# Kernel optimization log

Measured on AMD Instinct MI355X. Metric: run time of the kernel, lower is better.

Reference implementation:

```python
import jax, jax.numpy as jnp
import numpy as np
from jax import lax

B_, L_, D_ = 4, 512, 512          # batch, seq_len, in_dim (d_model)
HID, H2 = 512, 256                # hidden_dim, per-direction LSTM width
NL, DST, DCV, DIN, DTR = 3, 16, 4, 1024, 32  # layers, d_state, d_conv, d_inner, dt_rank


def _silu(x):
    return x * jax.nn.sigmoid(x)


def _layernorm(x, g, b):
    m = x.mean(-1, keepdims=True)
    v = x.var(-1, keepdims=True)
    return (x - m) / jnp.sqrt(v + 1e-5) * g + b


def _mamba(x, wi, cw, cb, xpw, dw, db, Alog, Dp, wo):
    # x: (B,L,D)
    Bsz, Ls, _ = x.shape
    xz = jnp.einsum('bld,ed->ble', x, wi)          # (B,L,2*DIN)
    xin, z = jnp.split(xz, 2, axis=-1)
    # causal depthwise conv1d (kernel DCV, left-padded)
    xpad = jnp.pad(xin, ((0, 0), (DCV - 1, 0), (0, 0)))
    u = cb + sum(xpad[:, k:k + Ls, :] * cw[:, k] for k in range(DCV))
    u = _silu(u)                                   # (B,L,DIN)
    xdbl = jnp.einsum('blc,ec->ble', u, xpw)       # (B,L,DTR+2*DST)
    dt_in = xdbl[..., :DTR]
    Bc = xdbl[..., DTR:DTR + DST]
    Cc = xdbl[..., DTR + DST:]
    dt = jax.nn.softplus(jnp.einsum('blr,cr->blc', dt_in, dw) + db)  # (B,L,DIN)
    A = -jnp.exp(Alog)                             # (DIN,DST), negative

    def step(h, inp):
        dt_t, B_t, C_t, u_t = inp                  # (B,DIN),(B,DST),(B,DST),(B,DIN)
        dA = jnp.exp(dt_t[..., None] * A)          # (B,DIN,DST)
        h = dA * h + (dt_t * u_t)[..., None] * B_t[:, None, :]
        y = jnp.einsum('bcn,bn->bc', h, C_t)
        return h, y

    h0 = jnp.zeros((Bsz, DIN, DST), x.dtype)
    _, ys = lax.scan(step, h0, (dt.transpose(1, 0, 2), Bc.transpose(1, 0, 2),
                                Cc.transpose(1, 0, 2), u.transpose(1, 0, 2)))
    y = ys.transpose(1, 0, 2) + u * Dp
    y = y * _silu(z)
    return jnp.einsum('blc,dc->bld', y, wo)


def _lstm_dir(x, wih, whh, bih, bhh, reverse):
    Bsz = x.shape[0]

    def step(carry, xt):
        h, c = carry
        g = xt @ wih.T + h @ whh.T + bih + bhh     # (B,4*H2), PyTorch gate order i,f,g,o
        i, f, gg, o = jnp.split(g, 4, axis=-1)
        c = jax.nn.sigmoid(f) * c + jax.nn.sigmoid(i) * jnp.tanh(gg)
        h = jax.nn.sigmoid(o) * jnp.tanh(c)
        return (h, c), h

    init = (jnp.zeros((Bsz, H2), x.dtype), jnp.zeros((Bsz, H2), x.dtype))
    _, hs = lax.scan(step, init, x.transpose(1, 0, 2), reverse=reverse)
    return hs.transpose(1, 0, 2)


def setup_inputs():
    key = jax.random.key(0)
    ks = jax.random.split(key, 16)
    rn = lambda k, s, sc=0.02: jax.random.normal(k, s, jnp.float32) * sc
    inp = {}
    inp['x'] = jax.random.normal(ks[0], (B_, L_, D_), jnp.float32)
    inp['in_proj_w'] = rn(ks[1], (NL, 2 * DIN, D_))
    inp['conv_w'] = rn(ks[2], (NL, DIN, DCV), 0.2)
    inp['conv_b'] = jnp.zeros((NL, DIN), jnp.float32)
    inp['x_proj_w'] = rn(ks[3], (NL, DTR + 2 * DST, DIN))
    inp['dt_proj_w'] = rn(ks[4], (NL, DIN, DTR), 0.1)
    inp['dt_proj_b'] = jnp.full((NL, DIN), -4.0, jnp.float32)
    inp['A_log'] = jnp.log(jnp.broadcast_to(jnp.arange(1, DST + 1, dtype=jnp.float32), (NL, DIN, DST)))
    inp['D_param'] = jnp.ones((NL, DIN), jnp.float32)
    inp['out_proj_w'] = rn(ks[5], (NL, D_, DIN))
    inp['ln_g'] = jnp.ones((NL, D_), jnp.float32)
    inp['ln_b'] = jnp.zeros((NL, D_), jnp.float32)
    inp['lstm_w_ih'] = rn(ks[6], (2, 4 * H2, D_), 0.05)
    inp['lstm_w_hh'] = rn(ks[7], (2, 4 * H2, H2), 0.05)
    inp['lstm_b_ih'] = jnp.zeros((2, 4 * H2), jnp.float32)
    inp['lstm_b_hh'] = jnp.zeros((2, 4 * H2), jnp.float32)
    inp['fusion_w'] = rn(ks[8], (HID, D_ + HID), 0.02)
    inp['fusion_b'] = jnp.zeros((HID,), jnp.float32)
    return inp


def reference(x, in_proj_w, conv_w, conv_b, x_proj_w, dt_proj_w, dt_proj_b, A_log,
              D_param, out_proj_w, ln_g, ln_b, lstm_w_ih, lstm_w_hh, lstm_b_ih,
              lstm_b_hh, fusion_w, fusion_b):
    m = x
    for i in range(NL):
        mo = _mamba(m, in_proj_w[i], conv_w[i], conv_b[i], x_proj_w[i],
                    dt_proj_w[i], dt_proj_b[i], A_log[i], D_param[i], out_proj_w[i])
        m = _layernorm(m + mo, ln_g[i], ln_b[i])
    lf = _lstm_dir(x, lstm_w_ih[0], lstm_w_hh[0], lstm_b_ih[0], lstm_b_hh[0], False)
    lb = _lstm_dir(x, lstm_w_ih[1], lstm_w_hh[1], lstm_b_ih[1], lstm_b_hh[1], True)
    comb = jnp.concatenate([m, lf, lb], axis=-1)   # (B,L,D_+HID)
    return comb @ fusion_w.T + fusion_b
```

## Files before the change

kernel.cpp:

```cpp
#include <hip/hip_runtime.h>
#include <math.h>

#define B_  4
#define L_  512
#define D_  512
#define DIN 1024
#define DST 16
#define DCV 4
#define DTR 32
#define NL  3
#define H2  256
#define LCH 64
#define NCH 8
#define WSC 0.28f

typedef _Float16 __f16;
typedef __f16 f16x2 __attribute__((ext_vector_type(2)));
typedef __f16 half8 __attribute__((ext_vector_type(8)));
typedef float f32x4v __attribute__((ext_vector_type(4)));
typedef unsigned uint4v __attribute__((ext_vector_type(4)));

__device__ __forceinline__ float fast_sigmoid(float x) { return 1.f / (1.f + __expf(-x)); }
__device__ __forceinline__ float fast_tanh(float x) { return 2.f / (1.f + __expf(-2.f * x)) - 1.f; }

__device__ __forceinline__ unsigned packf16(float a, float b) {
  f16x2 p; p.x = (__f16)a; p.y = (__f16)b;
  return __builtin_bit_cast(unsigned, p);
}
__device__ __forceinline__ int sdot4(unsigned a, unsigned b, int c) {
  return __builtin_amdgcn_sdot4((int)a, (int)b, c, false);
}
__device__ __forceinline__ int q8(float v) {
  float c = fmaxf(fminf(v, 127.f), -127.f);
  return (int)rintf(c);
}

template<int ACT, bool ACC, bool HOUT>
__global__ __launch_bounds__(256) void gemm_mfma_h(
    const __f16* __restrict__ A, const __f16* __restrict__ W, void* __restrict__ Cv,
    int M, int N, int K, int lda, int ldb, int ldc,
    const float* __restrict__ bias, const float* __restrict__ bias2)
{
  __shared__ uint4v As[1024];
  __shared__ uint4v Bs[1024];
  const int tid  = threadIdx.x;
  const int lane = tid & 63, wid = tid >> 6;
  const int wr = wid >> 1, wc = wid & 1;
  const int fr = lane & 15, fq = lane >> 4;
  const int m0 = blockIdx.y * 128, n0 = blockIdx.x * 128;
  const int srow = tid >> 3, skb = tid & 7;

  f32x4v acc[4][4] = {};
  for (int k0 = 0; k0 < K; k0 += 64) {
    const __f16* Ab = A + (size_t)m0 * lda + k0;
    const __f16* Bb = W + (size_t)n0 * ldb + k0;
    #pragma unroll
    for (int i = 0; i < 4; ++i) {
      int row = srow + i * 32;
      uint4v ap = *(const uint4v*)(Ab + (size_t)row * lda + skb * 8);
      uint4v bp = *(const uint4v*)(Bb + (size_t)row * ldb + skb * 8);
      As[row * 8 + (skb ^ (row & 7))] = ap;
      Bs[row * 8 + (skb ^ (row & 7))] = bp;
    }
    __syncthreads();
    #pragma unroll
    for (int ks = 0; ks < 2; ++ks) {
      half8 af[4], bf[4];
      #pragma unroll
      for (int mt = 0; mt < 4; ++mt) {
        int row = wr * 64 + mt * 16 + fr;
        int kb = ks * 4 + fq;
        af[mt] = __builtin_bit_cast(half8, As[row * 8 + (kb ^ (row & 7))]);
      }
      #pragma unroll
      for (int nt = 0; nt < 4; ++nt) {
        int row = wc * 64 + nt * 16 + fr;
        int kb = ks * 4 + fq;
        bf[nt] = __builtin_bit_cast(half8, Bs[row * 8 + (kb ^ (row & 7))]);
      }
      #pragma unroll
      for (int mt = 0; mt < 4; ++mt)
        #pragma unroll
        for (int nt = 0; nt < 4; ++nt)
          acc[mt][nt] = __builtin_amdgcn_mfma_f32_16x16x32_f16(af[mt], bf[nt], acc[mt][nt], 0, 0, 0);
    }
    __syncthreads();
  }
  float* C = (float*)Cv;
  __f16* Ch = (__f16*)Cv;
  #pragma unroll
  for (int nt = 0; nt < 4; ++nt) {
    int n = n0 + wc * 64 + nt * 16 + fr;
    float bv = (bias ? bias[n] : 0.f) + (bias2 ? bias2[n] : 0.f);
    #pragma unroll
    for (int mt = 0; mt < 4; ++mt) {
      #pragma unroll
      for (int r = 0; r < 4; ++r) {
        int m = m0 + wr * 64 + mt * 16 + fq * 4 + r;
        float v = acc[mt][nt][r] + bv;
        if (ACT == 1) v = (v > 20.f) ? v : log1pf(__expf(v));
        if (HOUT) Ch[(size_t)m * ldc + n] = (__f16)v;
        else if (ACC) C[(size_t)m * ldc + n] += v;
        else C[(size_t)m * ldc + n] = v;
      }
    }
  }
}

__global__ __launch_bounds__(256) void packh(
    const float* __restrict__ src, __f16* __restrict__ dst, int n)
{
  int t = blockIdx.x * 256 + threadIdx.x;
  if (t < n) dst[t] = (__f16)src[t];
}

__global__ __launch_bounds__(256) void pack_xpw_h(
    const float* __restrict__ xpw, __f16* __restrict__ dst)
{
  int t = blockIdx.x * 256 + threadIdx.x;
  int layer = t >> 17;
  int r = (t >> 10) & 127;
  int k = t & 1023;
  dst[t] = (r < 64) ? (__f16)xpw[layer * 65536 + r * 1024 + k] : (__f16)0.f;
}

__global__ __launch_bounds__(256) void pack_dwh(
    const float* __restrict__ dw, __f16* __restrict__ dst)
{
  int t = blockIdx.x * 256 + threadIdx.x;
  int layer = t >> 16;
  int r = (t >> 6) & 1023;
  int k = t & 63;
  dst[t] = (k < 32) ? (__f16)dw[layer * 32768 + r * 32 + k] : (__f16)0.f;
}

__global__ __launch_bounds__(256) void pack_whh_i8(
    const float* __restrict__ whh, uint4* __restrict__ dst)
{
  int idx = blockIdx.x * 256 + threadIdx.x;
  int t = idx & 511;
  int q = (idx >> 9) & 7;
  int r = idx >> 12;
  int G = r & 3, dir = r >> 2;
  int j = t >> 1, ks = t & 1;
  const float* src = whh + (size_t)dir * 262144 + (size_t)(G * 256 + j) * 256 + ks * 128 + q * 16;
  const float inv = 127.f / WSC;
  unsigned d[4];
  #pragma unroll
  for (int w = 0; w < 4; ++w) {
    float4 f = ((const float4*)src)[w];
    int q0 = q8(f.x * inv), q1 = q8(f.y * inv), q2 = q8(f.z * inv), q3 = q8(f.w * inv);
    d[w] = (unsigned)(q0 & 255) | ((unsigned)(q1 & 255) << 8) |
           ((unsigned)(q2 & 255) << 16) | ((unsigned)(q3 & 255) << 24);
  }
  uint4 pk; pk.x = d[0]; pk.y = d[1]; pk.z = d[2]; pk.w = d[3];
  dst[idx] = pk;
}

__global__ __launch_bounds__(256) void conv_silu(
    const float* __restrict__ xz, const float* __restrict__ cw, const float* __restrict__ cb,
    float* __restrict__ u, __f16* __restrict__ uh)
{
  int t = blockIdx.x * 256 + threadIdx.x;
  int c  = t & (DIN - 1);
  int bl = t >> 10;
  int l  = bl & (L_ - 1);
  float acc = cb[c];
  #pragma unroll
  for (int k = 0; k < DCV; ++k) {
    int ls = l + k - (DCV - 1);
    if (ls >= 0)
      acc = fmaf(xz[(size_t)(bl + k - (DCV - 1)) * 2048 + c], cw[c * DCV + k], acc);
  }
  float v = acc * fast_sigmoid(acc);
  u[t] = v;
  uh[t] = (__f16)v;
}

__global__ __launch_bounds__(256) void scan_part(
    const float* __restrict__ dt, const float* __restrict__ u,
    const __f16* __restrict__ xdh, const float* __restrict__ A_log,
    float* __restrict__ hend, float* __restrict__ Pp)
{
  int t = blockIdx.x * 256 + threadIdx.x;
  int n  = t & 15;
  int ch = (t >> 4) & 7;
  int bc = t >> 7;
  int c  = bc & (DIN - 1);
  int b  = bc >> 10;
  float Ac = -__expf(A_log[c * DST + n]);
  float h = 0.f, P = 1.f;
  const size_t row = (size_t)b * L_ + ch * LCH;

#define DECLP(i) float dtv##i, uv##i, Bn##i;
  DECLP(0) DECLP(1) DECLP(2) DECLP(3)
#define LOADP(i, l) { \
    const size_t nb_ = row + (l); \
    dtv##i = dt[nb_ * DIN + c]; \
    uv##i  = u [nb_ * DIN + c]; \
    Bn##i  = (float)xdh[nb_ * 128 + 32 + n]; }
#define STEPP(i) { \
    float dA_ = __expf(dtv##i * Ac); \
    h = fmaf(dA_, h, (dtv##i * uv##i) * Bn##i); \
    P *= dA_; }

  LOADP(0, 0) LOADP(1, 1) LOADP(2, 2) LOADP(3, 3)
  for (int l = 0; l < LCH - 4; l += 4) {
    STEPP(0) LOADP(0, l + 4)
    STEPP(1) LOADP(1, l + 5)
    STEPP(2) LOADP(2, l + 6)
    STEPP(3) LOADP(3, l + 7)
  }
  STEPP(0) STEPP(1) STEPP(2) STEPP(3)
#undef DECLP
#undef LOADP
#undef STEPP
  int flat = bc * 16 + n;
  hend[ch * 65536 + flat] = h;
  Pp[ch * 65536 + flat]   = P;
}

__global__ __launch_bounds__(256) void scan_fix(
    const float* __restrict__ dt, const float* __restrict__ u,
    const __f16* __restrict__ xdh, const float* __restrict__ xz,
    const float* __restrict__ A_log, const float* __restrict__ Dp,
    const float* __restrict__ hend, const float* __restrict__ Pp,
    __f16* __restrict__ y)
{
  int t = blockIdx.x * 256 + threadIdx.x;
  int n  = t & 15;
  int ch = (t >> 4) & 7;
  int bc = t >> 7;
  int c  = bc & (DIN - 1);
  int b  = bc >> 10;
  float Ac = -__expf(A_log[c * DST + n]);
  float Dc = Dp[c];
  const int flat = bc * 16 + n;
  float h = 0.f;
  for (int c2 = 0; c2 < ch; ++c2)
    h = fmaf(Pp[c2 * 65536 + flat], h, hend[c2 * 65536 + flat]);
  const size_t row = (size_t)b * L_ + ch * LCH;

#define DECLP(i) float dtv##i, uv##i, Bn##i, Cn##i, zv##i;
  DECLP(0) DECLP(1) DECLP(2) DECLP(3)
#define LOADP(i, l) { \
    const size_t nb_ = row + (l); \
    dtv##i = dt[nb_ * DIN + c]; \
    uv##i  = u [nb_ * DIN + c]; \
    Bn##i  = (float)xdh[nb_ * 128 + 32 + n]; \
    Cn##i  = (float)xdh[nb_ * 128 + 48 + n]; \
    zv##i  = xz[nb_ * 2048 + 1024 + c]; }
#define STEPP(i, l) { \
    float dA_ = __expf(dtv##i * Ac); \
    h = fmaf(dA_, h, (dtv##i * uv##i) * Bn##i); \
    float p_ = h * Cn##i; \
    p_ += __shfl_xor(p_, 1, 64); \
    p_ += __shfl_xor(p_, 2, 64); \
    p_ += __shfl_xor(p_, 4, 64); \
    p_ += __shfl_xor(p_, 8, 64); \
    if (n == 0) { \
      float yv_ = p_ + uv##i * Dc; \
      yv_ *= zv##i * fast_sigmoid(zv##i); \
      y[(row + (l)) * DIN + c] = (__f16)yv_; \
    } }

  LOADP(0, 0) LOADP(1, 1) LOADP(2, 2) LOADP(3, 3)
  for (int l = 0; l < LCH - 4; l += 4) {
    STEPP(0, l)     LOADP(0, l + 4)
    STEPP(1, l + 1) LOADP(1, l + 5)
    STEPP(2, l + 2) LOADP(2, l + 6)
    STEPP(3, l + 3) LOADP(3, l + 7)
  }
  STEPP(0, LCH - 4) STEPP(1, LCH - 3) STEPP(2, LCH - 2) STEPP(3, LCH - 1)
#undef DECLP
#undef LOADP
#undef STEPP
}

__global__ __launch_bounds__(64) void resid_ln(
    const float* __restrict__ a, const float* __restrict__ mo,
    const float* __restrict__ g, const float* __restrict__ bta,
    float* __restrict__ outm, int ldo, __f16* __restrict__ outh, int ldoh)
{
  int row = blockIdx.x;
  int lane = threadIdx.x;
  const float* pa = a  + (size_t)row * 512;
  const float* pb = mo + (size_t)row * 512;
  float v[8];
  float s = 0.f, s2 = 0.f;
  #pragma unroll
  for (int i = 0; i < 8; ++i) {
    float x = pa[lane + i * 64] + pb[lane + i * 64];
    v[i] = x; s += x; s2 += x * x;
  }
  #pragma unroll
  for (int off = 1; off < 64; off <<= 1) {
    s  += __shfl_xor(s,  off, 64);
    s2 += __shfl_xor(s2, off, 64);
  }
  float mean = s * (1.f / 512.f);
  float var  = s2 * (1.f / 512.f) - mean * mean;
  float rstd = rsqrtf(var + 1e-5f);
  #pragma unroll
  for (int i = 0; i < 8; ++i) {
    int cidx = lane + i * 64;
    float o = (v[i] - mean) * rstd * g[cidx] + bta[cidx];
    if (outm) outm[(size_t)row * ldo + cidx] = o;
    outh[(size_t)row * ldoh + cidx] = (__f16)o;
  }
}


#define W8STEP(q) { \
    uint4 hq = h8s[buf][(q)*2 + ks]; \
    uint4 wi_ = wp8[(0*8+(q))*512 + t]; \
    uint4 wf_ = wp8[(1*8+(q))*512 + t]; \
    uint4 wg = wg_lds[(q)*512 + t]; \
    uint4 wo = wo_lds[(q)*512 + t]; \
    ii_ = sdot4(wi_.x, hq.x, ii_); ii_ = sdot4(wi_.y, hq.y, ii_); \
    ii_ = sdot4(wi_.z, hq.z, ii_); ii_ = sdot4(wi_.w, hq.w, ii_); \
    if_ = sdot4(wf_.x, hq.x, if_); if_ = sdot4(wf_.y, hq.y, if_); \
    if_ = sdot4(wf_.z, hq.z, if_); if_ = sdot4(wf_.w, hq.w, if_); \
    ig_ = sdot4(wg.x, hq.x, ig_); ig_ = sdot4(wg.y, hq.y, ig_); \
    ig_ = sdot4(wg.z, hq.z, ig_); ig_ = sdot4(wg.w, hq.w, ig_); \
    io_ = sdot4(wo.x, hq.x, io_); io_ = sdot4(wo.y, hq.y, io_); \
    io_ = sdot4(wo.z, hq.z, io_); io_ = sdot4(wo.w, hq.w, io_); }
#define REP8(M) M(0) M(1) M(2) M(3) M(4) M(5) M(6) M(7)

__global__ __launch_bounds__(512, 1) void lstm_rec(
    const float* __restrict__ gx, const uint4* __restrict__ wpk8,
    __f16* __restrict__ comb)
{
  __shared__ uint4 wg_lds[8 * 512];
  __shared__ uint4 wo_lds[8 * 512];
  __shared__ __align__(16) uint4 h8s[2][16];
  const int dir = blockIdx.x >> 2, b = blockIdx.x & 3;
  const int t = threadIdx.x;
  const int j = t >> 1, ks = t & 1;
  const uint4* wp8 = wpk8 + (size_t)dir * 4 * 8 * 512;
  const float WS = WSC / (127.f * 127.f);

  #pragma unroll
  for (int q = 0; q < 8; ++q) {
    wg_lds[q * 512 + t] = wp8[(2 * 8 + q) * 512 + t];
    wo_lds[q * 512 + t] = wp8[(3 * 8 + q) * 512 + t];
  }

  if (t < 128) ((unsigned*)h8s)[t] = 0u;
  float c_reg = 0.f;
  __f16* outp = comb + 512 + dir * 256;
  const float* gxb = gx + (size_t)(b * L_) * 2048 + dir * 1024;
  const int offA = (ks ? 1 : 0) * 256 + j;
  const int offB = (ks ? 3 : 2) * 256 + j;
  const int d_   = t >> 3;
  const int ks8  = d_ >> 5;
  const int h8i  = (((d_ - ks8 * 32) >> 2) * 2 + ks8) * 4 + (d_ & 3);
  __syncthreads();

  int buf = 0;
  const int l0 = dir ? (L_ - 1) : 0;
  float pgA = gxb[(size_t)l0 * 2048 + offA];
  float pgB = gxb[(size_t)l0 * 2048 + offB];

  for (int s = 0; s < L_; ++s) {
    const int l = dir ? (L_ - 1 - s) : s;
    float pgA_n = 0.f, pgB_n = 0.f;
    if (s + 1 < L_) {
      const int ln = dir ? (L_ - 2 - s) : (s + 1);
      pgA_n = gxb[(size_t)ln * 2048 + offA];
      pgB_n = gxb[(size_t)ln * 2048 + offB];
    }
    int ii_ = 0, if_ = 0, ig_ = 0, io_ = 0;
    REP8(W8STEP)
    float a0 = (float)ii_ * WS;
    float a1 = (float)if_ * WS;
    float a2 = (float)ig_ * WS;
    float a3 = (float)io_ * WS;
    if (ks == 0) { a0 += pgA; a2 += pgB; } else { a1 += pgA; a3 += pgB; }
    a0 += __shfl_xor(a0, 1, 64);
    a1 += __shfl_xor(a1, 1, 64);
    a2 += __shfl_xor(a2, 1, 64);
    a3 += __shfl_xor(a3, 1, 64);
    const float si = fast_sigmoid(a0);
    const float sf = fast_sigmoid(a1);
    const float tg = fast_tanh(a2);
    const float so = fast_sigmoid(a3);
    c_reg = fmaf(sf, c_reg, si * tg);
    const float hv = so * fast_tanh(c_reg);
    if (ks == 0) outp[(size_t)(b * L_ + l) * 1024 + j] = (__f16)hv;
    const float hv1 = __shfl_xor(hv, 2, 64);
    const float hv2 = __shfl_xor(hv, 4, 64);
    const float hv3 = __shfl_xor(hv1, 4, 64);
    if ((t & 7) == 0) {
      int q0 = (int)rintf(hv  * 127.f), q1 = (int)rintf(hv1 * 127.f);
      int q2 = (int)rintf(hv2 * 127.f), q3 = (int)rintf(hv3 * 127.f);
      ((unsigned*)h8s[buf ^ 1])[h8i] =
          (unsigned)(q0 & 255) | ((unsigned)(q1 & 255) << 8) |
          ((unsigned)(q2 & 255) << 16) | ((unsigned)(q3 & 255) << 24);
    }
    pgA = pgA_n; pgB = pgB_n;
    buf ^= 1;
    __syncthreads();
  }
}

extern "C" void kernel_launch(void* const* d_in, const int* in_sizes, int n_in,
                              void* d_out, int out_size, void* d_ws, size_t ws_size,
                              hipStream_t stream)
{
  const float* x    = (const float*)d_in[0];
  const float* wi   = (const float*)d_in[1];
  const float* cw   = (const float*)d_in[2];
  const float* cb   = (const float*)d_in[3];
  const float* xpw  = (const float*)d_in[4];
  const float* dw   = (const float*)d_in[5];
  const float* db   = (const float*)d_in[6];
  const float* Alog = (const float*)d_in[7];
  const float* Dp   = (const float*)d_in[8];
  const float* wo   = (const float*)d_in[9];
  const float* lng  = (const float*)d_in[10];
  const float* lnb  = (const float*)d_in[11];
  const float* wih  = (const float*)d_in[12];
  const float* whh  = (const float*)d_in[13];
  const float* bih  = (const float*)d_in[14];
  const float* bhh  = (const float*)d_in[15];
  const float* fw   = (const float*)d_in[16];
  const float* fb   = (const float*)d_in[17];
  float* out = (float*)d_out;

  float* F = (float*)d_ws;
  float* xz     = F;
  float* gx     = F;
  float* mo     = F + 3145728;
  float* u      = F + 4194304;
  __f16* xdh    = (__f16*)(F + 7340032);
  float* dt     = F + 7602176;
  float* mbuf   = F + 10747904;
  __f16* fw_h   = (__f16*)(F + 4194304);
  __f16* u_h    = (__f16*)(F + 6291456);
  __f16* wih_h  = (__f16*)(F + 7602176);
  uint4* wpk8   = (uint4*)(F + 8126464);
  __f16* wi_hc  = (__f16*)(F + 8388608);
  float* hend   = F + 8388608;
  __f16* ybuf_h = (__f16*)(F + 9699328);
  __f16* x_h    = (__f16*)(F + 9699328);
  __f16* mbuf_h = (__f16*)(F + 11796480);
  float* Pp     = F + 11796480;
  __f16* comb_h = (__f16*)(F + 12320768);
  __f16* wo_h   = (__f16*)(F + 13369344);
  __f16* xpw_h  = (__f16*)(F + 14155776);
  __f16* dwh    = (__f16*)(F + 14352384);

  const int M = B_ * L_;
  dim3 blk(256);

  packh<<<dim3(4096), blk, 0, stream>>>(x,   x_h,   1048576);
  packh<<<dim3(4096), blk, 0, stream>>>(wih, wih_h, 1048576);
  packh<<<dim3(6144), blk, 0, stream>>>(wo,  wo_h,  1572864);
  pack_xpw_h<<<dim3(1536), blk, 0, stream>>>(xpw, xpw_h);
  pack_dwh<<<dim3(768), blk, 0, stream>>>(dw, dwh);

  gemm_mfma_h<0,false,false><<<dim3(16, 16), blk, 0, stream>>>(
      x_h, wih_h, gx, M, 2048, 512, 512, 512, 2048, bih, bhh);
  pack_whh_i8<<<dim3(128), blk, 0, stream>>>(whh, wpk8);
  lstm_rec<<<dim3(8), dim3(512), 0, stream>>>(gx, wpk8, comb_h);

  for (int i = 0; i < NL; ++i) {
    const float* min = (i == 0) ? x : mbuf;
    const __f16* min_h = (i == 0) ? x_h : mbuf_h;
    packh<<<dim3(4096), blk, 0, stream>>>(wi + (size_t)i*1048576, wi_hc, 1048576);
    gemm_mfma_h<0,false,false><<<dim3(16, 16), blk, 0, stream>>>(
        min_h, wi_hc, xz, M, 2048, 512, 512, 512, 2048, nullptr, nullptr);
    conv_silu<<<dim3(8192), blk, 0, stream>>>(
        xz, cw + (size_t)i*DIN*DCV, cb + i*DIN, u, u_h);
    gemm_mfma_h<0,false,true><<<dim3(1, 16), blk, 0, stream>>>(
        u_h, xpw_h + (size_t)i*131072, xdh, M, 128, 1024, 1024, 1024, 128, nullptr, nullptr);
    gemm_mfma_h<1,false,false><<<dim3(8, 16), blk, 0, stream>>>(
        xdh, dwh + (size_t)i*65536, dt, M, 1024, 64, 128, 64, 1024, db + i*1024, nullptr);
    scan_part<<<dim3(2048), blk, 0, stream>>>(
        dt, u, xdh, Alog + (size_t)i*DIN*DST, hend, Pp);
    scan_fix<<<dim3(2048), blk, 0, stream>>>(
        dt, u, xdh, xz, Alog + (size_t)i*DIN*DST, Dp + i*DIN, hend, Pp, ybuf_h);
    gemm_mfma_h<0,false,false><<<dim3(4, 16), blk, 0, stream>>>(
        ybuf_h, wo_h + (size_t)i*524288, mo, M, 512, 1024, 1024, 1024, 512, nullptr, nullptr);
    if (i < NL - 1)
      resid_ln<<<dim3(M), dim3(64), 0, stream>>>(
          min, mo, lng + i*512, lnb + i*512, mbuf, 512, mbuf_h, 512);
    else
      resid_ln<<<dim3(M), dim3(64), 0, stream>>>(
          min, mo, lng + i*512, lnb + i*512, nullptr, 0, comb_h, 1024);
  }

  packh<<<dim3(2048), blk, 0, stream>>>(fw, fw_h, 524288);
  gemm_mfma_h<0,false,false><<<dim3(4, 16), blk, 0, stream>>>(
      comb_h, fw_h, out, M, 512, 1024, 1024, 1024, 512, fb, nullptr);
}
```

Measured before the change: 1.273 ms.

## Split LSTM recurrence into segments co-scheduled inside Mamba GEMM launches

The serial LSTM recurrence, previously its own 8-block kernel, is split into 512 steps spread across 12 segments. Each segment runs as extra blocks appended to one of the Mamba GEMM launches, so the recurrence overlaps the GEMM tiles. The GEMMs become a 512-thread kernel computing two tiles per block, and LSTM c/h state is carried through global memory between launches. The input-gate projection and u are now stored as fp16, cutting bandwidth at some cost in precision. The added risk is per-segment cost to reload weights into LDS, plus the ordering assumption that launches on one stream run sequentially.

```diff
diff --git a/kernel.cpp b/kernel.cpp
--- a/kernel.cpp
+++ b/kernel.cpp
@@ -11,7 +11,6 @@
 #define NL  3
 #define H2  256
 #define LCH 64
-#define NCH 8
 #define WSC 0.28f
 
 typedef _Float16 __f16;
@@ -35,284 +34,46 @@
   return (int)rintf(c);
 }
 
-template<int ACT, bool ACC, bool HOUT>
-__global__ __launch_bounds__(256) void gemm_mfma_h(
-    const __f16* __restrict__ A, const __f16* __restrict__ W, void* __restrict__ Cv,
-    int M, int N, int K, int lda, int ldb, int ldc,
-    const float* __restrict__ bias, const float* __restrict__ bias2)
-{
-  __shared__ uint4v As[1024];
-  __shared__ uint4v Bs[1024];
-  const int tid  = threadIdx.x;
-  const int lane = tid & 63, wid = tid >> 6;
-  const int wr = wid >> 1, wc = wid & 1;
-  const int fr = lane & 15, fq = lane >> 4;
-  const int m0 = blockIdx.y * 128, n0 = blockIdx.x * 128;
-  const int srow = tid >> 3, skb = tid & 7;
-
-  f32x4v acc[4][4] = {};
-  for (int k0 = 0; k0 < K; k0 += 64) {
-    const __f16* Ab = A + (size_t)m0 * lda + k0;
-    const __f16* Bb = W + (size_t)n0 * ldb + k0;
-    #pragma unroll
-    for (int i = 0; i < 4; ++i) {
-      int row = srow + i * 32;
-      uint4v ap = *(const uint4v*)(Ab + (size_t)row * lda + skb * 8);
-      uint4v bp = *(const uint4v*)(Bb + (size_t)row * ldb + skb * 8);
-      As[row * 8 + (skb ^ (row & 7))] = ap;
-      Bs[row * 8 + (skb ^ (row & 7))] = bp;
-    }
-    __syncthreads();
-    #pragma unroll
-    for (int ks = 0; ks < 2; ++ks) {
-      half8 af[4], bf[4];
-      #pragma unroll
-      for (int mt = 0; mt < 4; ++mt) {
-        int row = wr * 64 + mt * 16 + fr;
-        int kb = ks * 4 + fq;
-        af[mt] = __builtin_bit_cast(half8, As[row * 8 + (kb ^ (row & 7))]);
-      }
-      #pragma unroll
-      for (int nt = 0; nt < 4; ++nt) {
-        int row = wc * 64 + nt * 16 + fr;
-        int kb = ks * 4 + fq;
-        bf[nt] = __builtin_bit_cast(half8, Bs[row * 8 + (kb ^ (row & 7))]);
-      }
-      #pragma unroll
-      for (int mt = 0; mt < 4; ++mt)
-        #pragma unroll
-        for (int nt = 0; nt < 4; ++nt)
-          acc[mt][nt] = __builtin_amdgcn_mfma_f32_16x16x32_f16(af[mt], bf[nt], acc[mt][nt], 0, 0, 0);
-    }
-    __syncthreads();
-  }
-  float* C = (float*)Cv;
-  __f16* Ch = (__f16*)Cv;
-  #pragma unroll
-  for (int nt = 0; nt < 4; ++nt) {
-    int n = n0 + wc * 64 + nt * 16 + fr;
-    float bv = (bias ? bias[n] : 0.f) + (bias2 ? bias2[n] : 0.f);
-    #pragma unroll
-    for (int mt = 0; mt < 4; ++mt) {
-      #pragma unroll
-      for (int r = 0; r < 4; ++r) {
-        int m = m0 + wr * 64 + mt * 16 + fq * 4 + r;
-        float v = acc[mt][nt][r] + bv;
-        if (ACT == 1) v = (v > 20.f) ? v : log1pf(__expf(v));
-        if (HOUT) Ch[(size_t)m * ldc + n] = (__f16)v;
-        else if (ACC) C[(size_t)m * ldc + n] += v;
-        else C[(size_t)m * ldc + n] = v;
-      }
-    }
-  }
-}
-
-__global__ __launch_bounds__(256) void packh(
-    const float* __restrict__ src, __f16* __restrict__ dst, int n)
-{
-  int t = blockIdx.x * 256 + threadIdx.x;
-  if (t < n) dst[t] = (__f16)src[t];
-}
-
-__global__ __launch_bounds__(256) void pack_xpw_h(
-    const float* __restrict__ xpw, __f16* __restrict__ dst)
-{
-  int t = blockIdx.x * 256 + threadIdx.x;
-  int layer = t >> 17;
-  int r = (t >> 10) & 127;
-  int k = t & 1023;
-  dst[t] = (r < 64) ? (__f16)xpw[layer * 65536 + r * 1024 + k] : (__f16)0.f;
-}
-
-__global__ __launch_bounds__(256) void pack_dwh(
-    const float* __restrict__ dw, __f16* __restrict__ dst)
-{
-  int t = blockIdx.x * 256 + threadIdx.x;
-  int layer = t >> 16;
-  int r = (t >> 6) & 1023;
-  int k = t & 63;
-  dst[t] = (k < 32) ? (__f16)dw[layer * 32768 + r * 32 + k] : (__f16)0.f;
-}
-
-__global__ __launch_bounds__(256) void pack_whh_i8(
-    const float* __restrict__ whh, uint4* __restrict__ dst)
-{
-  int idx = blockIdx.x * 256 + threadIdx.x;
-  int t = idx & 511;
-  int q = (idx >> 9) & 7;
-  int r = idx >> 12;
-  int G = r & 3, dir = r >> 2;
-  int j = t >> 1, ks = t & 1;
-  const float* src = whh + (size_t)dir * 262144 + (size_t)(G * 256 + j) * 256 + ks * 128 + q * 16;
-  const float inv = 127.f / WSC;
-  unsigned d[4];
-  #pragma unroll
-  for (int w = 0; w < 4; ++w) {
-    float4 f = ((const float4*)src)[w];
-    int q0 = q8(f.x * inv), q1 = q8(f.y * inv), q2 = q8(f.z * inv), q3 = q8(f.w * inv);
-    d[w] = (unsigned)(q0 & 255) | ((unsigned)(q1 & 255) << 8) |
-           ((unsigned)(q2 & 255) << 16) | ((unsigned)(q3 & 255) << 24);
-  }
-  uint4 pk; pk.x = d[0]; pk.y = d[1]; pk.z = d[2]; pk.w = d[3];
-  dst[idx] = pk;
-}
-
-__global__ __launch_bounds__(256) void conv_silu(
-    const float* __restrict__ xz, const float* __restrict__ cw, const float* __restrict__ cb,
-    float* __restrict__ u, __f16* __restrict__ uh)
-{
-  int t = blockIdx.x * 256 + threadIdx.x;
-  int c  = t & (DIN - 1);
-  int bl = t >> 10;
-  int l  = bl & (L_ - 1);
-  float acc = cb[c];
-  #pragma unroll
-  for (int k = 0; k < DCV; ++k) {
-    int ls = l + k - (DCV - 1);
-    if (ls >= 0)
-      acc = fmaf(xz[(size_t)(bl + k - (DCV - 1)) * 2048 + c], cw[c * DCV + k], acc);
-  }
-  float v = acc * fast_sigmoid(acc);
-  u[t] = v;
-  uh[t] = (__f16)v;
-}
-
-__global__ __launch_bounds__(256) void scan_part(
-    const float* __restrict__ dt, const float* __restrict__ u,
-    const __f16* __restrict__ xdh, const float* __restrict__ A_log,
-    float* __restrict__ hend, float* __restrict__ Pp)
-{
-  int t = blockIdx.x * 256 + threadIdx.x;
-  int n  = t & 15;
-  int ch = (t >> 4) & 7;
-  int bc = t >> 7;
-  int c  = bc & (DIN - 1);
-  int b  = bc >> 10;
-  float Ac = -__expf(A_log[c * DST + n]);
-  float h = 0.f, P = 1.f;
-  const size_t row = (size_t)b * L_ + ch * LCH;
-
-#define DECLP(i) float dtv##i, uv##i, Bn##i;
-  DECLP(0) DECLP(1) DECLP(2) DECLP(3)
-#define LOADP(i, l) { \
-    const size_t nb_ = row + (l); \
-    dtv##i = dt[nb_ * DIN + c]; \
-    uv##i  = u [nb_ * DIN + c]; \
-    Bn##i  = (float)xdh[nb_ * 128 + 32 + n]; }
-#define STEPP(i) { \
-    float dA_ = __expf(dtv##i * Ac); \
-    h = fmaf(dA_, h, (dtv##i * uv##i) * Bn##i); \
-    P *= dA_; }
-
-  LOADP(0, 0) LOADP(1, 1) LOADP(2, 2) LOADP(3, 3)
-  for (int l = 0; l < LCH - 4; l += 4) {
-    STEPP(0) LOADP(0, l + 4)
-    STEPP(1) LOADP(1, l + 5)
-    STEPP(2) LOADP(2, l + 6)
-    STEPP(3) LOADP(3, l + 7)
-  }
-  STEPP(0) STEPP(1) STEPP(2) STEPP(3)
-#undef DECLP
-#undef LOADP
-#undef STEPP
-  int flat = bc * 16 + n;
-  hend[ch * 65536 + flat] = h;
-  Pp[ch * 65536 + flat]   = P;
-}
-
-__global__ __launch_bounds__(256) void scan_fix(
-    const float* __restrict__ dt, const float* __restrict__ u,
-    const __f16* __restrict__ xdh, const float* __restrict__ xz,
-    const float* __restrict__ A_log, const float* __restrict__ Dp,
-    const float* __restrict__ hend, const float* __restrict__ Pp,
-    __f16* __restrict__ y)
-{
-  int t = blockIdx.x * 256 + threadIdx.x;
-  int n  = t & 15;
-  int ch = (t >> 4) & 7;
-  int bc = t >> 7;
-  int c  = bc & (DIN - 1);
-  int b  = bc >> 10;
-  float Ac = -__expf(A_log[c * DST + n]);
-  float Dc = Dp[c];
-  const int flat = bc * 16 + n;
-  float h = 0.f;
-  for (int c2 = 0; c2 < ch; ++c2)
-    h = fmaf(Pp[c2 * 65536 + flat], h, hend[c2 * 65536 + flat]);
-  const size_t row = (size_t)b * L_ + ch * LCH;
-
-#define DECLP(i) float dtv##i, uv##i, Bn##i, Cn##i, zv##i;
-  DECLP(0) DECLP(1) DECLP(2) DECLP(3)
-#define LOADP(i, l) { \
-    const size_t nb_ = row + (l); \
-    dtv##i = dt[nb_ * DIN + c]; \
-    uv##i  = u [nb_ * DIN + c]; \
-    Bn##i  = (float)xdh[nb_ * 128 + 32 + n]; \
-    Cn##i  = (float)xdh[nb_ * 128 + 48 + n]; \
-    zv##i  = xz[nb_ * 2048 + 1024 + c]; }
-#define STEPP(i, l) { \
-    float dA_ = __expf(dtv##i * Ac); \
-    h = fmaf(dA_, h, (dtv##i * uv##i) * Bn##i); \
-    float p_ = h * Cn##i; \
-    p_ += __shfl_xor(p_, 1, 64); \
-    p_ += __shfl_xor(p_, 2, 64); \
-    p_ += __shfl_xor(p_, 4, 64); \
-    p_ += __shfl_xor(p_, 8, 64); \
-    if (n == 0) { \
-      float yv_ = p_ + uv##i * Dc; \
-      yv_ *= zv##i * fast_sigmoid(zv##i); \
-      y[(row + (l)) * DIN + c] = (__f16)yv_; \
-    } }
-
-  LOADP(0, 0) LOADP(1, 1) LOADP(2, 2) LOADP(3, 3)
-  for (int l = 0; l < LCH - 4; l += 4) {
-    STEPP(0, l)     LOADP(0, l + 4)
-    STEPP(1, l + 1) LOADP(1, l + 5)
-    STEPP(2, l + 2) LOADP(2, l + 6)
-    STEPP(3, l + 3) LOADP(3, l + 7)
-  }
-  STEPP(0, LCH - 4) STEPP(1, LCH - 3) STEPP(2, LCH - 2) STEPP(3, LCH - 1)
-#undef DECLP
-#undef LOADP
-#undef STEPP
-}
-
-__global__ __launch_bounds__(64) void resid_ln(
-    const float* __restrict__ a, const float* __restrict__ mo,
-    const float* __restrict__ g, const float* __restrict__ bta,
-    float* __restrict__ outm, int ldo, __f16* __restrict__ outh, int ldoh)
-{
-  int row = blockIdx.x;
-  int lane = threadIdx.x;
-  const float* pa = a  + (size_t)row * 512;
-  const float* pb = mo + (size_t)row * 512;
-  float v[8];
-  float s = 0.f, s2 = 0.f;
-  #pragma unroll
-  for (int i = 0; i < 8; ++i) {
-    float x = pa[lane + i * 64] + pb[lane + i * 64];
-    v[i] = x; s += x; s2 += x * x;
-  }
-  #pragma unroll
-  for (int off = 1; off < 64; off <<= 1) {
-    s  += __shfl_xor(s,  off, 64);
-    s2 += __shfl_xor(s2, off, 64);
-  }
-  float mean = s * (1.f / 512.f);
-  float var  = s2 * (1.f / 512.f) - mean * mean;
-  float rstd = rsqrtf(var + 1e-5f);
-  #pragma unroll
-  for (int i = 0; i < 8; ++i) {
-    int cidx = lane + i * 64;
-    float o = (v[i] - mean) * rstd * g[cidx] + bta[cidx];
-    if (outm) outm[(size_t)row * ldo + cidx] = o;
-    outh[(size_t)row * ldoh + cidx] = (__f16)o;
-  }
-}
-
+__device__ void lstm_seg(char* smem, const __f16* gxh, const uint4* wpk8,
+                         __f16* comb, float* c_state, uint4* h8_state,
+                         int s0, int s1, int lb)
+{
+  uint4* wg_lds = (uint4*)smem;
+  uint4* wo_lds = wg_lds + 8 * 512;
+  uint4* h8s    = wo_lds + 8 * 512;
+  const int dir = lb >> 2, b = lb & 3;
+  const int t = threadIdx.x;
+  const int j = t >> 1, ks = t & 1;
+  const uint4* wp8 = wpk8 + (size_t)dir * 4 * 8 * 512;
+  const float WS = WSC / (127.f * 127.f);
+
+  #pragma unroll
+  for (int q = 0; q < 8; ++q) {
+    wg_lds[q * 512 + t] = wp8[(2 * 8 + q) * 512 + t];
+    wo_lds[q * 512 + t] = wp8[(3 * 8 + q) * 512 + t];
+  }
+  int buf = s0 & 1;
+  if (s0 == 0) {
+    if (t < 128) ((unsigned*)h8s)[t] = 0u;
+  } else {
+    if (t < 64) ((unsigned*)h8s)[buf * 64 + t] = ((const unsigned*)(h8_state + lb * 16))[t];
+  }
+  float c_reg = (s0 == 0) ? 0.f : c_state[lb * 512 + t];
+  __f16* outp = comb + 512 + dir * 256;
+  const __f16* gxb = gxh + (size_t)(b * L_) * 2048 + dir * 1024;
+  const int offA = (ks ? 1 : 0) * 256 + j;
+  const int offB = (ks ? 3 : 2) * 256 + j;
+  const int d_   = t >> 3;
+  const int ks8  = d_ >> 5;
+  const int h8i  = (((d_ - ks8 * 32) >> 2) * 2 + ks8) * 4 + (d_ & 3);
+  __syncthreads();
+
+  const int l00 = dir ? (L_ - 1 - s0) : s0;
+  float pgA = (float)gxb[(size_t)l00 * 2048 + offA];
+  float pgB = (float)gxb[(size_t)l00 * 2048 + offB];
 
 #define W8STEP(q) { \
-    uint4 hq = h8s[buf][(q)*2 + ks]; \
+    uint4 hq = h8s[buf * 16 + (q) * 2 + ks]; \
     uint4 wi_ = wp8[(0*8+(q))*512 + t]; \
     uint4 wf_ = wp8[(1*8+(q))*512 + t]; \
     uint4 wg = wg_lds[(q)*512 + t]; \
@@ -325,53 +86,18 @@
     ig_ = sdot4(wg.z, hq.z, ig_); ig_ = sdot4(wg.w, hq.w, ig_); \
     io_ = sdot4(wo.x, hq.x, io_); io_ = sdot4(wo.y, hq.y, io_); \
     io_ = sdot4(wo.z, hq.z, io_); io_ = sdot4(wo.w, hq.w, io_); }
-#define REP8(M) M(0) M(1) M(2) M(3) M(4) M(5) M(6) M(7)
-
-__global__ __launch_bounds__(512, 1) void lstm_rec(
-    const float* __restrict__ gx, const uint4* __restrict__ wpk8,
-    __f16* __restrict__ comb)
-{
-  __shared__ uint4 wg_lds[8 * 512];
-  __shared__ uint4 wo_lds[8 * 512];
-  __shared__ __align__(16) uint4 h8s[2][16];
-  const int dir = blockIdx.x >> 2, b = blockIdx.x & 3;
-  const int t = threadIdx.x;
-  const int j = t >> 1, ks = t & 1;
-  const uint4* wp8 = wpk8 + (size_t)dir * 4 * 8 * 512;
-  const float WS = WSC / (127.f * 127.f);
-
-  #pragma unroll
-  for (int q = 0; q < 8; ++q) {
-    wg_lds[q * 512 + t] = wp8[(2 * 8 + q) * 512 + t];
-    wo_lds[q * 512 + t] = wp8[(3 * 8 + q) * 512 + t];
-  }
-
-  if (t < 128) ((unsigned*)h8s)[t] = 0u;
-  float c_reg = 0.f;
-  __f16* outp = comb + 512 + dir * 256;
-  const float* gxb = gx + (size_t)(b * L_) * 2048 + dir * 1024;
-  const int offA = (ks ? 1 : 0) * 256 + j;
-  const int offB = (ks ? 3 : 2) * 256 + j;
-  const int d_   = t >> 3;
-  const int ks8  = d_ >> 5;
-  const int h8i  = (((d_ - ks8 * 32) >> 2) * 2 + ks8) * 4 + (d_ & 3);
-  __syncthreads();
-
-  int buf = 0;
-  const int l0 = dir ? (L_ - 1) : 0;
-  float pgA = gxb[(size_t)l0 * 2048 + offA];
-  float pgB = gxb[(size_t)l0 * 2048 + offB];
-
-  for (int s = 0; s < L_; ++s) {
+
+  for (int s = s0; s < s1; ++s) {
     const int l = dir ? (L_ - 1 - s) : s;
     float pgA_n = 0.f, pgB_n = 0.f;
     if (s + 1 < L_) {
       const int ln = dir ? (L_ - 2 - s) : (s + 1);
-      pgA_n = gxb[(size_t)ln * 2048 + offA];
-      pgB_n = gxb[(size_t)ln * 2048 + offB];
+      pgA_n = (float)gxb[(size_t)ln * 2048 + offA];
+      pgB_n = (float)gxb[(size_t)ln * 2048 + offB];
     }
     int ii_ = 0, if_ = 0, ig_ = 0, io_ = 0;
-    REP8(W8STEP)
+    W8STEP(0) W8STEP(1) W8STEP(2) W8STEP(3)
+    W8STEP(4) W8STEP(5) W8STEP(6) W8STEP(7)
     float a0 = (float)ii_ * WS;
     float a1 = (float)if_ * WS;
     float a2 = (float)ig_ * WS;
@@ -394,13 +120,372 @@
     if ((t & 7) == 0) {
       int q0 = (int)rintf(hv  * 127.f), q1 = (int)rintf(hv1 * 127.f);
       int q2 = (int)rintf(hv2 * 127.f), q3 = (int)rintf(hv3 * 127.f);
-      ((unsigned*)h8s[buf ^ 1])[h8i] =
+      ((unsigned*)(h8s + (buf ^ 1) * 16))[h8i] =
           (unsigned)(q0 & 255) | ((unsigned)(q1 & 255) << 8) |
           ((unsigned)(q2 & 255) << 16) | ((unsigned)(q3 & 255) << 24);
     }
     pgA = pgA_n; pgB = pgB_n;
     buf ^= 1;
     __syncthreads();
+  }
+#undef W8STEP
+  if (t < 64) ((unsigned*)(h8_state + lb * 16))[t] = ((unsigned*)(h8s + (s1 & 1) * 16))[t];
+  c_state[lb * 512 + t] = c_reg;
+}
+
+template<int ACT, bool HOUT>
+__global__ __launch_bounds__(512, 1) void gemm512(
+    const __f16* __restrict__ A, const __f16* __restrict__ W, void* __restrict__ Cv,
+    int nx, int M, int N, int K, int lda, int ldb, int ldc,
+    const float* __restrict__ bias,
+    int tileBlocks,
+    const __f16* __restrict__ gxh, const uint4* __restrict__ wpk8,
+    __f16* __restrict__ comb, float* __restrict__ c_state, uint4* __restrict__ h8_state,
+    int s0, int s1)
+{
+  extern __shared__ char smem[];
+  if ((int)blockIdx.x >= tileBlocks) {
+    lstm_seg(smem, gxh, wpk8, comb, c_state, h8_state, s0, s1, (int)blockIdx.x - tileBlocks);
+    return;
+  }
+  const int half = threadIdx.x >> 8;
+  const int tid  = threadIdx.x & 255;
+  const int tile = (int)blockIdx.x * 2 + half;
+  const int tx = tile % nx, ty = tile / nx;
+  uint4v* As = (uint4v*)(smem + half * 32768);
+  uint4v* Bs = As + 1024;
+  const int lane = tid & 63, wid = tid >> 6;
+  const int wr = wid >> 1, wc = wid & 1;
+  const int fr = lane & 15, fq = lane >> 4;
+  const int m0 = ty * 128, n0 = tx * 128;
+  const int srow = tid >> 3, skb = tid & 7;
+
+  f32x4v acc[4][4] = {};
+  for (int k0 = 0; k0 < K; k0 += 64) {
+    const __f16* Ab = A + (size_t)m0 * lda + k0;
+    const __f16* Bb = W + (size_t)n0 * ldb + k0;
+    #pragma unroll
+    for (int i = 0; i < 4; ++i) {
+      int row = srow + i * 32;
+      uint4v ap = *(const uint4v*)(Ab + (size_t)row * lda + skb * 8);
+      uint4v bp = *(const uint4v*)(Bb + (size_t)row * ldb + skb * 8);
+      As[row * 8 + (skb ^ (row & 7))] = ap;
+      Bs[row * 8 + (skb ^ (row & 7))] = bp;
+    }
+    __syncthreads();
+    #pragma unroll
+    for (int ks = 0; ks < 2; ++ks) {
+      half8 af[4], bf[4];
+      #pragma unroll
+      for (int mt = 0; mt < 4; ++mt) {
+        int row = wr * 64 + mt * 16 + fr;
+        int kb = ks * 4 + fq;
+        af[mt] = __builtin_bit_cast(half8, As[row * 8 + (kb ^ (row & 7))]);
+      }
+      #pragma unroll
+      for (int nt = 0; nt < 4; ++nt) {
+        int row = wc * 64 + nt * 16 + fr;
+        int kb = ks * 4 + fq;
+        bf[nt] = __builtin_bit_cast(half8, Bs[row * 8 + (kb ^ (row & 7))]);
+      }
+      #pragma unroll
+      for (int mt = 0; mt < 4; ++mt)
+        #pragma unroll
+        for (int nt = 0; nt < 4; ++nt)
+          acc[mt][nt] = __builtin_amdgcn_mfma_f32_16x16x32_f16(af[mt], bf[nt], acc[mt][nt], 0, 0, 0);
+    }
+    __syncthreads();
+  }
+  float* C = (float*)Cv;
+  __f16* Ch = (__f16*)Cv;
+  #pragma unroll
+  for (int nt = 0; nt < 4; ++nt) {
+    int n = n0 + wc * 64 + nt * 16 + fr;
+    float bv = bias ? bias[n] : 0.f;
+    #pragma unroll
+    for (int mt = 0; mt < 4; ++mt) {
+      #pragma unroll
+      for (int r = 0; r < 4; ++r) {
+        int m = m0 + wr * 64 + mt * 16 + fq * 4 + r;
+        float v = acc[mt][nt][r] + bv;
+        if (ACT == 1) v = (v > 20.f) ? v : log1pf(__expf(v));
+        if (HOUT) Ch[(size_t)m * ldc + n] = (__f16)v;
+        else C[(size_t)m * ldc + n] = v;
+      }
+    }
+  }
+}
+
+template<int ACT, bool HOUT>
+__global__ __launch_bounds__(256) void gemm_mfma_h(
+    const __f16* __restrict__ A, const __f16* __restrict__ W, void* __restrict__ Cv,
+    int M, int N, int K, int lda, int ldb, int ldc,
+    const float* __restrict__ bias, const float* __restrict__ bias2)
+{
+  __shared__ uint4v As[1024];
+  __shared__ uint4v Bs[1024];
+  const int tid  = threadIdx.x;
+  const int lane = tid & 63, wid = tid >> 6;
+  const int wr = wid >> 1, wc = wid & 1;
+  const int fr = lane & 15, fq = lane >> 4;
+  const int m0 = blockIdx.y * 128, n0 = blockIdx.x * 128;
+  const int srow = tid >> 3, skb = tid & 7;
+
+  f32x4v acc[4][4] = {};
+  for (int k0 = 0; k0 < K; k0 += 64) {
+    const __f16* Ab = A + (size_t)m0 * lda + k0;
+    const __f16* Bb = W + (size_t)n0 * ldb + k0;
+    #pragma unroll
+    for (int i = 0; i < 4; ++i) {
+      int row = srow + i * 32;
+      uint4v ap = *(const uint4v*)(Ab + (size_t)row * lda + skb * 8);
+      uint4v bp = *(const uint4v*)(Bb + (size_t)row * ldb + skb * 8);
+      As[row * 8 + (skb ^ (row & 7))] = ap;
+      Bs[row * 8 + (skb ^ (row & 7))] = bp;
+    }
+    __syncthreads();
+    #pragma unroll
+    for (int ks = 0; ks < 2; ++ks) {
+      half8 af[4], bf[4];
+      #pragma unroll
+      for (int mt = 0; mt < 4; ++mt) {
+        int row = wr * 64 + mt * 16 + fr;
+        int kb = ks * 4 + fq;
+        af[mt] = __builtin_bit_cast(half8, As[row * 8 + (kb ^ (row & 7))]);
+      }
+      #pragma unroll
+      for (int nt = 0; nt < 4; ++nt) {
+        int row = wc * 64 + nt * 16 + fr;
+        int kb = ks * 4 + fq;
+        bf[nt] = __builtin_bit_cast(half8, Bs[row * 8 + (kb ^ (row & 7))]);
+      }
+      #pragma unroll
+      for (int mt = 0; mt < 4; ++mt)
+        #pragma unroll
+        for (int nt = 0; nt < 4; ++nt)
+          acc[mt][nt] = __builtin_amdgcn_mfma_f32_16x16x32_f16(af[mt], bf[nt], acc[mt][nt], 0, 0, 0);
+    }
+    __syncthreads();
+  }
+  float* C = (float*)Cv;
+  __f16* Ch = (__f16*)Cv;
+  #pragma unroll
+  for (int nt = 0; nt < 4; ++nt) {
+    int n = n0 + wc * 64 + nt * 16 + fr;
+    float bv = (bias ? bias[n] : 0.f) + (bias2 ? bias2[n] : 0.f);
+    #pragma unroll
+    for (int mt = 0; mt < 4; ++mt) {
+      #pragma unroll
+      for (int r = 0; r < 4; ++r) {
+        int m = m0 + wr * 64 + mt * 16 + fq * 4 + r;
+        float v = acc[mt][nt][r] + bv;
+        if (ACT == 1) v = (v > 20.f) ? v : log1pf(__expf(v));
+        if (HOUT) Ch[(size_t)m * ldc + n] = (__f16)v;
+        else C[(size_t)m * ldc + n] = v;
+      }
+    }
+  }
+}
+
+__global__ __launch_bounds__(256) void packh(
+    const float* __restrict__ src, __f16* __restrict__ dst, int n)
+{
+  int t = blockIdx.x * 256 + threadIdx.x;
+  if (t < n) dst[t] = (__f16)src[t];
+}
+
+__global__ __launch_bounds__(256) void pack_xpw_h(
+    const float* __restrict__ xpw, __f16* __restrict__ dst)
+{
+  int t = blockIdx.x * 256 + threadIdx.x;
+  int layer = t >> 17;
+  int r = (t >> 10) & 127;
+  int k = t & 1023;
+  dst[t] = (r < 64) ? (__f16)xpw[layer * 65536 + r * 1024 + k] : (__f16)0.f;
+}
+
+__global__ __launch_bounds__(256) void pack_dwh(
+    const float* __restrict__ dw, __f16* __restrict__ dst)
+{
+  int t = blockIdx.x * 256 + threadIdx.x;
+  int layer = t >> 16;
+  int r = (t >> 6) & 1023;
+  int k = t & 63;
+  dst[t] = (k < 32) ? (__f16)dw[layer * 32768 + r * 32 + k] : (__f16)0.f;
+}
+
+__global__ __launch_bounds__(256) void pack_whh_i8(
+    const float* __restrict__ whh, uint4* __restrict__ dst)
+{
+  int idx = blockIdx.x * 256 + threadIdx.x;
+  int t = idx & 511;
+  int q = (idx >> 9) & 7;
+  int r = idx >> 12;
+  int G = r & 3, dir = r >> 2;
+  int j = t >> 1, ks = t & 1;
+  const float* src = whh + (size_t)dir * 262144 + (size_t)(G * 256 + j) * 256 + ks * 128 + q * 16;
+  const float inv = 127.f / WSC;
+  unsigned d[4];
+  #pragma unroll
+  for (int w = 0; w < 4; ++w) {
+    float4 f = ((const float4*)src)[w];
+    int q0 = q8(f.x * inv), q1 = q8(f.y * inv), q2 = q8(f.z * inv), q3 = q8(f.w * inv);
+    d[w] = (unsigned)(q0 & 255) | ((unsigned)(q1 & 255) << 8) |
+           ((unsigned)(q2 & 255) << 16) | ((unsigned)(q3 & 255) << 24);
+  }
+  uint4 pk; pk.x = d[0]; pk.y = d[1]; pk.z = d[2]; pk.w = d[3];
+  dst[idx] = pk;
+}
+
+__global__ __launch_bounds__(256) void conv_silu(
+    const float* __restrict__ xz, const float* __restrict__ cw, const float* __restrict__ cb,
+    __f16* __restrict__ uh)
+{
+  int t = blockIdx.x * 256 + threadIdx.x;
+  int c  = t & (DIN - 1);
+  int bl = t >> 10;
+  int l  = bl & (L_ - 1);
+  float acc = cb[c];
+  #pragma unroll
+  for (int k = 0; k < DCV; ++k) {
+    int ls = l + k - (DCV - 1);
+    if (ls >= 0)
+      acc = fmaf(xz[(size_t)(bl + k - (DCV - 1)) * 2048 + c], cw[c * DCV + k], acc);
+  }
+  float v = acc * fast_sigmoid(acc);
+  uh[t] = (__f16)v;
+}
+
+__global__ __launch_bounds__(256) void scan_part(
+    const float* __restrict__ dt, const __f16* __restrict__ uh,
+    const __f16* __restrict__ xdh, const float* __restrict__ A_log,
+    float* __restrict__ hend, float* __restrict__ Pp)
+{
+  int t = blockIdx.x * 256 + threadIdx.x;
+  int n  = t & 15;
+  int ch = (t >> 4) & 7;
+  int bc = t >> 7;
+  int c  = bc & (DIN - 1);
+  int b  = bc >> 10;
+  float Ac = -__expf(A_log[c * DST + n]);
+  float h = 0.f, P = 1.f;
+  const size_t row = (size_t)b * L_ + ch * LCH;
+
+#define DECLP(i) float dtv##i, uv##i, Bn##i;
+  DECLP(0) DECLP(1) DECLP(2) DECLP(3)
+#define LOADP(i, l) { \
+    const size_t nb_ = row + (l); \
+    dtv##i = dt[nb_ * DIN + c]; \
+    uv##i  = (float)uh[nb_ * DIN + c]; \
+    Bn##i  = (float)xdh[nb_ * 128 + 32 + n]; }
+#define STEPP(i) { \
+    float dA_ = __expf(dtv##i * Ac); \
+    h = fmaf(dA_, h, (dtv##i * uv##i) * Bn##i); \
+    P *= dA_; }
+
+  LOADP(0, 0) LOADP(1, 1) LOADP(2, 2) LOADP(3, 3)
+  for (int l = 0; l < LCH - 4; l += 4) {
+    STEPP(0) LOADP(0, l + 4)
+    STEPP(1) LOADP(1, l + 5)
+    STEPP(2) LOADP(2, l + 6)
+    STEPP(3) LOADP(3, l + 7)
+  }
+  STEPP(0) STEPP(1) STEPP(2) STEPP(3)
+#undef DECLP
+#undef LOADP
+#undef STEPP
+  int flat = bc * 16 + n;
+  hend[ch * 65536 + flat] = h;
+  Pp[ch * 65536 + flat]   = P;
+}
+
+__global__ __launch_bounds__(256) void scan_fix(
+    const float* __restrict__ dt, const __f16* __restrict__ uh,
+    const __f16* __restrict__ xdh, const float* __restrict__ xz,
+    const float* __restrict__ A_log, const float* __restrict__ Dp,
+    const float* __restrict__ hend, const float* __restrict__ Pp,
+    __f16* __restrict__ y)
+{
+  int t = blockIdx.x * 256 + threadIdx.x;
+  int n  = t & 15;
+  int ch = (t >> 4) & 7;
+  int bc = t >> 7;
+  int c  = bc & (DIN - 1);
+  int b  = bc >> 10;
+  float Ac = -__expf(A_log[c * DST + n]);
+  float Dc = Dp[c];
+  const int flat = bc * 16 + n;
+  float h = 0.f;
+  for (int c2 = 0; c2 < ch; ++c2)
+    h = fmaf(Pp[c2 * 65536 + flat], h, hend[c2 * 65536 + flat]);
+  const size_t row = (size_t)b * L_ + ch * LCH;
+
+#define DECLP(i) float dtv##i, uv##i, Bn##i, Cn##i, zv##i;
+  DECLP(0) DECLP(1) DECLP(2) DECLP(3)
+#define LOADP(i, l) { \
+    const size_t nb_ = row + (l); \
+    dtv##i = dt[nb_ * DIN + c]; \
+    uv##i  = (float)uh[nb_ * DIN + c]; \
+    Bn##i  = (float)xdh[nb_ * 128 + 32 + n]; \
+    Cn##i  = (float)xdh[nb_ * 128 + 48 + n]; \
+    zv##i  = xz[nb_ * 2048 + 1024 + c]; }
+#define STEPP(i, l) { \
+    float dA_ = __expf(dtv##i * Ac); \
+    h = fmaf(dA_, h, (dtv##i * uv##i) * Bn##i); \
+    float p_ = h * Cn##i; \
+    p_ += __shfl_xor(p_, 1, 64); \
+    p_ += __shfl_xor(p_, 2, 64); \
+    p_ += __shfl_xor(p_, 4, 64); \
+    p_ += __shfl_xor(p_, 8, 64); \
+    if (n == 0) { \
+      float yv_ = p_ + uv##i * Dc; \
+      yv_ *= zv##i * fast_sigmoid(zv##i); \
+      y[(row + (l)) * DIN + c] = (__f16)yv_; \
+    } }
+
+  LOADP(0, 0) LOADP(1, 1) LOADP(2, 2) LOADP(3, 3)
+  for (int l = 0; l < LCH - 4; l += 4) {
+    STEPP(0, l)     LOADP(0, l + 4)
+    STEPP(1, l + 1) LOADP(1, l + 5)
+    STEPP(2, l + 2) LOADP(2, l + 6)
+    STEPP(3, l + 3) LOADP(3, l + 7)
+  }
+  STEPP(0, LCH - 4) STEPP(1, LCH - 3) STEPP(2, LCH - 2) STEPP(3, LCH - 1)
+#undef DECLP
+#undef LOADP
+#undef STEPP
+}
+
+__global__ __launch_bounds__(64) void resid_ln(
+    const float* __restrict__ a, const float* __restrict__ mo,
+    const float* __restrict__ g, const float* __restrict__ bta,
+    float* __restrict__ outm, int ldo, __f16* __restrict__ outh, int ldoh)
+{
+  int row = blockIdx.x;
+  int lane = threadIdx.x;
+  const float* pa = a  + (size_t)row * 512;
+  const float* pb = mo + (size_t)row * 512;
+  float v[8];
+  float s = 0.f, s2 = 0.f;
+  #pragma unroll
+  for (int i = 0; i < 8; ++i) {
+    float x = pa[lane + i * 64] + pb[lane + i * 64];
+    v[i] = x; s += x; s2 += x * x;
+  }
+  #pragma unroll
+  for (int off = 1; off < 64; off <<= 1) {
+    s  += __shfl_xor(s,  off, 64);
+    s2 += __shfl_xor(s2, off, 64);
+  }
+  float mean = s * (1.f / 512.f);
+  float var  = s2 * (1.f / 512.f) - mean * mean;
+  float rstd = rsqrtf(var + 1e-5f);
+  #pragma unroll
+  for (int i = 0; i < 8; ++i) {
+    int cidx = lane + i * 64;
+    float o = (v[i] - mean) * rstd * g[cidx] + bta[cidx];
+    if (outm) outm[(size_t)row * ldo + cidx] = o;
+    outh[(size_t)row * ldoh + cidx] = (__f16)o;
   }
 }
 
@@ -430,16 +515,14 @@
 
   float* F = (float*)d_ws;
   float* xz     = F;
-  float* gx     = F;
   float* mo     = F + 3145728;
-  float* u      = F + 4194304;
+  __f16* gxh    = (__f16*)(F + 4194304);
+  __f16* u_h    = (__f16*)(F + 6291456);
   __f16* xdh    = (__f16*)(F + 7340032);
   float* dt     = F + 7602176;
   float* mbuf   = F + 10747904;
   __f16* fw_h   = (__f16*)(F + 4194304);
-  __f16* u_h    = (__f16*)(F + 6291456);
   __f16* wih_h  = (__f16*)(F + 7602176);
-  uint4* wpk8   = (uint4*)(F + 8126464);
   __f16* wi_hc  = (__f16*)(F + 8388608);
   float* hend   = F + 8388608;
   __f16* ybuf_h = (__f16*)(F + 9699328);
@@ -450,39 +533,54 @@
   __f16* wo_h   = (__f16*)(F + 13369344);
   __f16* xpw_h  = (__f16*)(F + 14155776);
   __f16* dwh    = (__f16*)(F + 14352384);
+  float* c_state = F + 14450688;
+  uint4* h8_state = (uint4*)(F + 14454784);
+  uint4* wpk8   = (uint4*)(F + 14455296);
 
   const int M = B_ * L_;
   dim3 blk(256);
+  const size_t LSH = 132096;
 
   packh<<<dim3(4096), blk, 0, stream>>>(x,   x_h,   1048576);
   packh<<<dim3(4096), blk, 0, stream>>>(wih, wih_h, 1048576);
   packh<<<dim3(6144), blk, 0, stream>>>(wo,  wo_h,  1572864);
   pack_xpw_h<<<dim3(1536), blk, 0, stream>>>(xpw, xpw_h);
   pack_dwh<<<dim3(768), blk, 0, stream>>>(dw, dwh);
-
-  gemm_mfma_h<0,false,false><<<dim3(16, 16), blk, 0, stream>>>(
-      x_h, wih_h, gx, M, 2048, 512, 512, 512, 2048, bih, bhh);
   pack_whh_i8<<<dim3(128), blk, 0, stream>>>(whh, wpk8);
-  lstm_rec<<<dim3(8), dim3(512), 0, stream>>>(gx, wpk8, comb_h);
+
+  gemm_mfma_h<0,true><<<dim3(16, 16), blk, 0, stream>>>(
+      x_h, wih_h, gxh, M, 2048, 512, 512, 512, 2048, bih, bhh);
+
+  int scur = 0;
+  auto nb = [&](int n) { int a = scur; scur += n; return a; };
 
   for (int i = 0; i < NL; ++i) {
     const float* min = (i == 0) ? x : mbuf;
     const __f16* min_h = (i == 0) ? x_h : mbuf_h;
     packh<<<dim3(4096), blk, 0, stream>>>(wi + (size_t)i*1048576, wi_hc, 1048576);
-    gemm_mfma_h<0,false,false><<<dim3(16, 16), blk, 0, stream>>>(
-        min_h, wi_hc, xz, M, 2048, 512, 512, 512, 2048, nullptr, nullptr);
+    { int s0 = nb(43);
+      gemm512<0,false><<<dim3(136), dim3(512), LSH, stream>>>(
+        min_h, wi_hc, xz, 16, M, 2048, 512, 512, 512, 2048, nullptr,
+        128, gxh, wpk8, comb_h, c_state, h8_state, s0, s0 + 43); }
     conv_silu<<<dim3(8192), blk, 0, stream>>>(
-        xz, cw + (size_t)i*DIN*DCV, cb + i*DIN, u, u_h);
-    gemm_mfma_h<0,false,true><<<dim3(1, 16), blk, 0, stream>>>(
-        u_h, xpw_h + (size_t)i*131072, xdh, M, 128, 1024, 1024, 1024, 128, nullptr, nullptr);
-    gemm_mfma_h<1,false,false><<<dim3(8, 16), blk, 0, stream>>>(
-        xdh, dwh + (size_t)i*65536, dt, M, 1024, 64, 128, 64, 1024, db + i*1024, nullptr);
+        xz, cw + (size_t)i*DIN*DCV, cb + i*DIN, u_h);
+    { int s0 = nb(43);
+      gemm512<0,true><<<dim3(16), dim3(512), LSH, stream>>>(
+        u_h, xpw_h + (size_t)i*131072, xdh, 1, M, 128, 1024, 1024, 1024, 128, nullptr,
+        8, gxh, wpk8, comb_h, c_state, h8_state, s0, s0 + 43); }
+    { int s0 = nb(43);
+      gemm512<1,false><<<dim3(72), dim3(512), LSH, stream>>>(
+        xdh, dwh + (size_t)i*65536, dt, 8, M, 1024, 64, 128, 64, 1024, db + i*1024,
+        64, gxh, wpk8, comb_h, c_state, h8_state, s0, s0 + 43); }
     scan_part<<<dim3(2048), blk, 0, stream>>>(
-        dt, u, xdh, Alog + (size_t)i*DIN*DST, hend, Pp);
+        dt, u_h, xdh, Alog + (size_t)i*DIN*DST, hend, Pp);
     scan_fix<<<dim3(2048), blk, 0, stream>>>(
-        dt, u, xdh, xz, Alog + (size_t)i*DIN*DST, Dp + i*DIN, hend, Pp, ybuf_h);
-    gemm_mfma_h<0,false,false><<<dim3(4, 16), blk, 0, stream>>>(
-        ybuf_h, wo_h + (size_t)i*524288, mo, M, 512, 1024, 1024, 1024, 512, nullptr, nullptr);
+        dt, u_h, xdh, xz, Alog + (size_t)i*DIN*DST, Dp + i*DIN, hend, Pp, ybuf_h);
+    { int cnt = (i == NL - 1) ? 39 : 43;
+      int s0 = nb(cnt);
+      gemm512<0,false><<<dim3(40), dim3(512), LSH, stream>>>(
+        ybuf_h, wo_h + (size_t)i*524288, mo, 4, M, 512, 1024, 1024, 1024, 512, nullptr,
+        32, gxh, wpk8, comb_h, c_state, h8_state, s0, s0 + cnt); }
     if (i < NL - 1)
       resid_ln<<<dim3(M), dim3(64), 0, stream>>>(
           min, mo, lng + i*512, lnb + i*512, mbuf, 512, mbuf_h, 512);
@@ -492,6 +590,6 @@
   }
 
   packh<<<dim3(2048), blk, 0, stream>>>(fw, fw_h, 524288);
-  gemm_mfma_h<0,false,false><<<dim3(4, 16), blk, 0, stream>>>(
+  gemm_mfma_h<0,false><<<dim3(4, 16), blk, 0, stream>>>(
       comb_h, fw_h, out, M, 512, 1024, 1024, 1024, 512, fb, nullptr);
 }
```

Result: slower. 1.604 ms (+25.9%).
